# Performance work log

Hardware: AMD Instinct MI355X
Metric: run time of the kernel (lower is better)

## Reference

```python
import jax, jax.numpy as jnp
import numpy as np

B, T, D, H, C = 32, 2048, 64, 512, 10


def setup_inputs() -> dict:
    key = jax.random.key(0)
    ks = jax.random.split(key, 7)
    s_ih = 1.0 / np.sqrt(H)
    return {
        "x": jax.random.normal(ks[0], (B, T, D), dtype=jnp.float32),
        # PyTorch GRU params: gates ordered (r, z, n)
        "w_ih": jax.random.uniform(ks[1], (3 * H, D), jnp.float32, -s_ih, s_ih),
        "w_hh": jax.random.uniform(ks[2], (3 * H, H), jnp.float32, -s_ih, s_ih),
        "b_ih": jax.random.uniform(ks[3], (3 * H,), jnp.float32, -s_ih, s_ih),
        "b_hh": jax.random.uniform(ks[4], (3 * H,), jnp.float32, -s_ih, s_ih),
        "w_fc": jax.random.uniform(ks[5], (C, H), jnp.float32, -s_ih, s_ih),
        "b_fc": jax.random.uniform(ks[6], (C,), jnp.float32, -s_ih, s_ih),
    }


def _gru_seq(x, w_ih, w_hh, b_ih, b_hh):
    # Precompute input-to-hidden gates for all timesteps: [B,T,3H] -> [T,B,3H]
    gx = jnp.einsum("btd,gd->btg", x, w_ih) + b_ih
    gx = jnp.swapaxes(gx, 0, 1)
    h0 = jnp.zeros((x.shape[0], w_hh.shape[1]), dtype=x.dtype)

    def step(h, gxt):
        gh = h @ w_hh.T + b_hh  # [B,3H]
        gx_r, gx_z, gx_n = jnp.split(gxt, 3, axis=-1)
        gh_r, gh_z, gh_n = jnp.split(gh, 3, axis=-1)
        r = jax.nn.sigmoid(gx_r + gh_r)
        z = jax.nn.sigmoid(gx_z + gh_z)
        n = jnp.tanh(gx_n + r * gh_n)
        h_new = (1.0 - z) * n + z * h
        return h_new, h_new

    _, hs = jax.lax.scan(step, h0, gx)  # hs: [T,B,H]
    return jnp.swapaxes(hs, 0, 1)  # [B,T,H]


def reference(x, w_ih, w_hh, b_ih, b_hh, w_fc, b_fc):
    out = _gru_seq(x, w_ih, w_hh, b_ih, b_hh)
    return jnp.einsum("bth,ch->btc", out, w_fc) + b_fc
```

## Files before the change

### kernel.cpp

```cpp
#include <hip/hip_runtime.h>
#include <cstdint>
#include <cstddef>

#define Bsz 32
#define Tn  2048
#define Dn  64
#define Hn  512
#define Cn  10
#define NDOM 16
#define NGB  16
#define UG   32
#define BPG  2
#define NTH  1024
#define RW   1024
#define PSTR 68

__device__ __forceinline__ float sigmoidf_(float v) { return 1.f / (1.f + __expf(-v)); }
__device__ __forceinline__ float tanhf_(float v) {
  const float c = fminf(fmaxf(v, -15.f), 15.f);
  const float e = __expf(-2.f * c);
  return (1.f - e) / (1.f + e);
}


__global__ __launch_bounds__(NTH) void gru_main(
    const float* __restrict__ x, const float* __restrict__ w_ih,
    const float* __restrict__ w_hh, const float* __restrict__ b_ih,
    const float* __restrict__ b_hh, float* __restrict__ hs,
    unsigned long long* __restrict__ xch)
{
  const int dom  = blockIdx.x & (NDOM - 1);
  const int g    = blockIdx.x >> 4;
  const int tid  = threadIdx.x;
  const int wave = tid >> 6;
  const int lane = tid & 63;
  const int u    = tid & 31;
  const int ksec = tid >> 5;

  __shared__ float hTb[2][1024];
  __shared__ float xT[2][128];
  __shared__ float part[64 * PSTR];

  float wreg[3][16];
  float wxreg[3][2];
  float brz0 = 0.f, brz1 = 0.f, bnx = 0.f, bnh = 0.f;
  #pragma unroll
  for (int i = 0; i < 3; ++i) {
    const int grow = i * Hn + g * UG + u;
    const float4* wp = (const float4*)(w_hh + (size_t)grow * Hn + ksec * 16);
    #pragma unroll
    for (int q = 0; q < 4; ++q) {
      const float4 v = wp[q];
      wreg[i][q * 4 + 0] = v.x; wreg[i][q * 4 + 1] = v.y;
      wreg[i][q * 4 + 2] = v.z; wreg[i][q * 4 + 3] = v.w;
    }
    wxreg[i][0] = w_ih[(size_t)grow * Dn + ksec * 2 + 0];
    wxreg[i][1] = w_ih[(size_t)grow * Dn + ksec * 2 + 1];
    if (i == 0) brz0 = b_ih[grow] + b_hh[grow];
    else if (i == 1) brz1 = b_ih[grow] + b_hh[grow];
    else { bnx = b_ih[grow]; bnh = b_hh[grow]; }
  }

  unsigned long long* const sl0 = xch + (size_t)dom * RW;
  unsigned long long* const sl1 = xch + (size_t)(NDOM + dom) * RW;

  const bool dopoll = (wave < 15);
  int wword = 0;
  if (dopoll) {
    const int idx = wave * 64 + lane;
    wword = (idx < g * 64) ? idx : idx + 64;
  }
  const int ownw = g * 64 + (lane & 31) * 2 + (lane >> 5);

  hTb[0][tid & 1023] = 0.f;
  if (tid < 128) {
    const int bp = tid >> 6, d = tid & 63;
    xT[0][d * 2 + bp] = x[((size_t)(dom * BPG + bp) * Tn + 0) * Dn + d];
  }
  float hold = 0.f;
  __syncthreads();

  for (int t = 0; t < Tn; ++t) {
    const int tp = t & 1;
    float* const hT = hTb[tp];
    unsigned long long* const slot = tp ? sl0 : sl1;

    const unsigned long long want = (unsigned long long)t;
    unsigned long long v = 0;
    if (t > 0 && dopoll)
      v = __hip_atomic_load(slot + wword, __ATOMIC_RELAXED, __HIP_MEMORY_SCOPE_AGENT);

    float xpre = 0.f;
    if (tid < 128) {
      const int bp = tid >> 6, d = tid & 63;
      const int tn = (t + 1 < Tn) ? (t + 1) : t;
      xpre = x[((size_t)(dom * BPG + bp) * Tn + tn) * Dn + d];
    }

    float acc[4][2];
    #pragma unroll
    for (int i = 0; i < 4; ++i) { acc[i][0] = 0.f; acc[i][1] = 0.f; }
    #pragma unroll
    for (int dd = 0; dd < 2; ++dd) {
      const float2 xb = *(const float2*)&xT[tp][(ksec * 2 + dd) * 2];
      #pragma unroll
      for (int i = 0; i < 3; ++i) {
        const float w = wxreg[i][dd];
        const int gi = (i == 2) ? 2 : i;
        acc[gi][0] += w * xb.x; acc[gi][1] += w * xb.y;
      }
    }

    if (dopoll) {
      if (t > 0) {
        int gd = 0;
        while ((v >> 32) != want) {
          v = __hip_atomic_load(slot + wword, __ATOMIC_RELAXED, __HIP_MEMORY_SCOPE_AGENT);
          if (++gd > (1 << 17)) break;
        }
        union { unsigned u32; float f; } c;
        c.u32 = (unsigned)v;
        hT[wword] = c.f;
      }
    } else if (t > 0) {
      const float4* pp = (const float4*)&part[lane * PSTR];
      float4 s = pp[0];
      #pragma unroll
      for (int w = 1; w < 16; ++w) {
        const float4 pv = pp[w];
        s.x += pv.x; s.y += pv.y; s.z += pv.z; s.w += pv.w;
      }
      const float r = sigmoidf_(s.x + brz0);
      const float z = sigmoidf_(s.y + brz1);
      const float n = tanhf_(s.z + bnx + r * (s.w + bnh));
      const float h = (1.f - z) * n + z * hold;
      hold = h;
      hT[ownw] = h;
      union { float f; unsigned u32; } cu; cu.f = h;
      asm volatile("s_waitcnt vmcnt(0)" ::: "memory");
      const unsigned long long w64 = (want << 32) | cu.u32;
      __hip_atomic_store(slot + ownw, w64, __ATOMIC_RELAXED, __HIP_MEMORY_SCOPE_AGENT);
      hs[((size_t)(t - 1) * NDOM + dom) * RW + ownw] = h;
    }

    if (tid < 128) { const int bp = tid >> 6, d = tid & 63; xT[tp ^ 1][d * 2 + bp] = xpre; }

    asm volatile("s_waitcnt lgkmcnt(0)" ::: "memory");
    __builtin_amdgcn_s_barrier();
    asm volatile("" ::: "memory");

    {
      const float* hp = hT + ksec * 32;
      #pragma unroll
      for (int k2 = 0; k2 < 8; ++k2) {
        const float4 hv = *(const float4*)(hp + k2 * 4);
        const float a0 = wreg[0][k2 * 2], a1 = wreg[0][k2 * 2 + 1];
        const float b0 = wreg[1][k2 * 2], b1 = wreg[1][k2 * 2 + 1];
        const float c0 = wreg[2][k2 * 2], c1 = wreg[2][k2 * 2 + 1];
        acc[0][0] += a0 * hv.x; acc[0][1] += a0 * hv.y;
        acc[0][0] += a1 * hv.z; acc[0][1] += a1 * hv.w;
        acc[1][0] += b0 * hv.x; acc[1][1] += b0 * hv.y;
        acc[1][0] += b1 * hv.z; acc[1][1] += b1 * hv.w;
        acc[3][0] += c0 * hv.x; acc[3][1] += c0 * hv.y;
        acc[3][0] += c1 * hv.z; acc[3][1] += c1 * hv.w;
      }
    }

    #pragma unroll
    for (int i = 0; i < 4; ++i) {
      acc[i][0] += __shfl_xor(acc[i][0], 32);
      acc[i][1] += __shfl_xor(acc[i][1], 32);
    }

    if (lane < 32) {
      float4 p0, p1;
      p0.x = acc[0][0]; p0.y = acc[1][0]; p0.z = acc[2][0]; p0.w = acc[3][0];
      p1.x = acc[0][1]; p1.y = acc[1][1]; p1.z = acc[2][1]; p1.w = acc[3][1];
      *(float4*)&part[u * PSTR + wave * 4]        = p0;
      *(float4*)&part[(32 + u) * PSTR + wave * 4] = p1;
    }

    asm volatile("s_waitcnt lgkmcnt(0)" ::: "memory");
    __builtin_amdgcn_s_barrier();
    asm volatile("" ::: "memory");
  }

  if (wave == 15) {
    const float4* pp = (const float4*)&part[lane * PSTR];
    float4 s = pp[0];
    #pragma unroll
    for (int w = 1; w < 16; ++w) {
      const float4 pv = pp[w];
      s.x += pv.x; s.y += pv.y; s.z += pv.z; s.w += pv.w;
    }
    const float r = sigmoidf_(s.x + brz0);
    const float z = sigmoidf_(s.y + brz1);
    const float n = tanhf_(s.z + bnx + r * (s.w + bnh));
    const float h = (1.f - z) * n + z * hold;
    hs[((size_t)(Tn - 1) * NDOM + dom) * RW + ownw] = h;
  }
}

__global__ __launch_bounds__(256) void gru_fc(const float* __restrict__ hs,
    const float* __restrict__ w_fc, const float* __restrict__ b_fc,
    float* __restrict__ out)
{
  __shared__ float wfc[Cn * Hn];
  const int tid = threadIdx.x;
  for (int i = tid; i < Cn * Hn; i += 256) wfc[i] = w_fc[i];
  __syncthreads();
  const int wave = tid >> 6, lane = tid & 63;
  const int bt = blockIdx.x * 4 + wave;
  const int b = bt >> 11, t = bt & (Tn - 1);
  const int dom = b >> 1, bp = b & 1;
  const float* src = hs + ((size_t)t * NDOM + dom) * RW;
  float acc[Cn];
  #pragma unroll
  for (int c = 0; c < Cn; ++c) acc[c] = 0.f;
  #pragma unroll
  for (int it = 0; it < 8; ++it) {
    const int unit = it * 64 + lane;
    const float h = src[unit * 2 + bp];
    #pragma unroll
    for (int c = 0; c < Cn; ++c) acc[c] += h * wfc[c * Hn + unit];
  }
  #pragma unroll
  for (int c = 0; c < Cn; ++c) {
    #pragma unroll
    for (int m = 1; m < 64; m <<= 1) acc[c] += __shfl_xor(acc[c], m);
  }
  if (lane == 0) {
    #pragma unroll
    for (int c = 0; c < Cn; ++c) out[(size_t)bt * Cn + c] = acc[c] + b_fc[c];
  }
}

__global__ __launch_bounds__(512) void gru_fallback(
    const float* __restrict__ x, const float* __restrict__ w_ih,
    const float* __restrict__ w_hh, const float* __restrict__ b_ih,
    const float* __restrict__ b_hh, const float* __restrict__ w_fc,
    const float* __restrict__ b_fc, float* __restrict__ out)
{
  const int b = blockIdx.x;
  const int tid = threadIdx.x;
  __shared__ float hsh[Hn];
  __shared__ float xsh[Dn];
  hsh[tid] = 0.f;
  __syncthreads();
  for (int t = 0; t < Tn; ++t) {
    if (tid < Dn) xsh[tid] = x[((size_t)b * Tn + t) * Dn + tid];
    __syncthreads();
    const int u = tid;
    float gxr = 0.f, gxz = 0.f, gxn = 0.f;
    for (int d = 0; d < Dn; ++d) {
      const float xv = xsh[d];
      gxr += w_ih[(size_t)u * Dn + d] * xv;
      gxz += w_ih[(size_t)(Hn + u) * Dn + d] * xv;
      gxn += w_ih[(size_t)(2 * Hn + u) * Dn + d] * xv;
    }
    float ghr = 0.f, ghz = 0.f, ghn = 0.f;
    for (int k = 0; k < Hn; ++k) {
      const float hv = hsh[k];
      ghr += w_hh[(size_t)u * Hn + k] * hv;
      ghz += w_hh[(size_t)(Hn + u) * Hn + k] * hv;
      ghn += w_hh[(size_t)(2 * Hn + u) * Hn + k] * hv;
    }
    const float r = sigmoidf_(gxr + b_ih[u] + ghr + b_hh[u]);
    const float z = sigmoidf_(gxz + b_ih[Hn + u] + ghz + b_hh[Hn + u]);
    const float n = tanhf(gxn + b_ih[2 * Hn + u] + r * (ghn + b_hh[2 * Hn + u]));
    const float hold = hsh[u];
    __syncthreads();
    hsh[u] = (1.f - z) * n + z * hold;
    __syncthreads();
    if (tid < 320) {
      const int c = tid >> 5, l = tid & 31;
      float a = 0.f;
      for (int kk = 0; kk < 16; ++kk) {
        const int j = l * 16 + kk;
        a += hsh[j] * w_fc[c * Hn + j];
      }
      a += __shfl_xor(a, 1); a += __shfl_xor(a, 2); a += __shfl_xor(a, 4);
      a += __shfl_xor(a, 8); a += __shfl_xor(a, 16);
      if (l == 0) out[((size_t)b * Tn + t) * Cn + c] = a + b_fc[c];
    }
    __syncthreads();
  }
}

extern "C" void kernel_launch(void* const* d_in, const int* in_sizes, int n_in,
                              void* d_out, int out_size, void* d_ws, size_t ws_size,
                              hipStream_t stream) {
  const float* x    = (const float*)d_in[0];
  const float* w_ih = (const float*)d_in[1];
  const float* w_hh = (const float*)d_in[2];
  const float* b_ih = (const float*)d_in[3];
  const float* b_hh = (const float*)d_in[4];
  const float* w_fc = (const float*)d_in[5];
  const float* b_fc = (const float*)d_in[6];
  float* out = (float*)d_out;

  const size_t hs_bytes  = (size_t)Tn * NDOM * RW * sizeof(float);
  const size_t xch_bytes = (size_t)2 * NDOM * RW * sizeof(unsigned long long);

  if (ws_size >= hs_bytes) {
    float* hs = (float*)d_ws;
    unsigned long long* xchg = (unsigned long long*)d_out;
    hipMemsetAsync(xchg, 0, xch_bytes, stream);
    hipLaunchKernelGGL(gru_main, dim3(NDOM * NGB), dim3(NTH), 0, stream,
                       x, w_ih, w_hh, b_ih, b_hh, hs, xchg);
    hipLaunchKernelGGL(gru_fc, dim3((Bsz * Tn) / 4), dim3(256), 0, stream,
                       hs, w_fc, b_fc, out);
  } else {
    hipLaunchKernelGGL(gru_fallback, dim3(Bsz), dim3(512), 0, stream,
                       x, w_ih, w_hh, b_ih, b_hh, w_fc, b_fc, out);
  }
}
```

Before: 5.479 ms.

## Merge two per-step barriers into one by double-buffering partials

The GRU recurrence loop now uses a single block barrier per timestep instead of two. Partial gate sums are double-buffered in shared memory, and the hidden vector goes to one shared buffer. Wave 15 reduces the previous step's partials and publishes its own h slice first, then every wave, including wave 15, polls global memory for the full h vector. This shortens the serial critical path per step but depends on subtle ordering: hT is rewritten without a barrier separating it from the previous step's reads, so there is a risk of races.

```diff
diff --git a/kernel.cpp b/kernel.cpp
--- a/kernel.cpp
+++ b/kernel.cpp
@@ -13,7 +13,6 @@
 #define BPG  2
 #define NTH  1024
 #define RW   1024
-#define PSTR 68
 
 __device__ __forceinline__ float sigmoidf_(float v) { return 1.f / (1.f + __expf(-v)); }
 __device__ __forceinline__ float tanhf_(float v) {
@@ -37,9 +36,9 @@
   const int u    = tid & 31;
   const int ksec = tid >> 5;
 
-  __shared__ float hTb[2][1024];
+  __shared__ float hT[1024];
   __shared__ float xT[2][128];
-  __shared__ float part[64 * PSTR];
+  __shared__ float part[2][4096];
 
   float wreg[3][16];
   float wxreg[3][2];
@@ -64,31 +63,46 @@
   unsigned long long* const sl0 = xch + (size_t)dom * RW;
   unsigned long long* const sl1 = xch + (size_t)(NDOM + dom) * RW;
 
-  const bool dopoll = (wave < 15);
-  int wword = 0;
-  if (dopoll) {
-    const int idx = wave * 64 + lane;
-    wword = (idx < g * 64) ? idx : idx + 64;
-  }
-  const int ownw = g * 64 + (lane & 31) * 2 + (lane >> 5);
-
-  hTb[0][tid & 1023] = 0.f;
+  const int wword = wave * 64 + lane;
+  const int ownw  = g * 64 + (lane & 31) * 2 + (lane >> 5);
+
+  hT[tid] = 0.f;
   if (tid < 128) {
     const int bp = tid >> 6, d = tid & 63;
     xT[0][d * 2 + bp] = x[((size_t)(dom * BPG + bp) * Tn + 0) * Dn + d];
   }
-  float hold = 0.f;
+  float hold = 0.f, hsave = 0.f;
   __syncthreads();
 
   for (int t = 0; t < Tn; ++t) {
     const int tp = t & 1;
-    float* const hT = hTb[tp];
     unsigned long long* const slot = tp ? sl0 : sl1;
-
     const unsigned long long want = (unsigned long long)t;
+
     unsigned long long v = 0;
-    if (t > 0 && dopoll)
+    if (t > 0) {
+      if (wave == 15) {
+        const float* pb = part[tp ^ 1];
+        float s0 = 0.f, s1 = 0.f, s2 = 0.f, s3 = 0.f;
+        #pragma unroll
+        for (int w = 0; w < 16; ++w) {
+          s0 += pb[       w * 64 + lane];
+          s1 += pb[1024 + w * 64 + lane];
+          s2 += pb[2048 + w * 64 + lane];
+          s3 += pb[3072 + w * 64 + lane];
+        }
+        const float r = sigmoidf_(s0 + brz0);
+        const float z = sigmoidf_(s1 + brz1);
+        const float n = tanhf_(s2 + bnx + r * (s3 + bnh));
+        const float h = (1.f - z) * n + z * hold;
+        hold = h; hsave = h;
+        union { float f; unsigned u32; } cu; cu.f = h;
+        asm volatile("s_waitcnt vmcnt(0)" ::: "memory");
+        __hip_atomic_store(slot + ownw, (want << 32) | cu.u32,
+                           __ATOMIC_RELAXED, __HIP_MEMORY_SCOPE_AGENT);
+      }
       v = __hip_atomic_load(slot + wword, __ATOMIC_RELAXED, __HIP_MEMORY_SCOPE_AGENT);
+    }
 
     float xpre = 0.f;
     if (tid < 128) {
@@ -111,43 +125,19 @@
       }
     }
 
-    if (dopoll) {
-      if (t > 0) {
-        int gd = 0;
-        while ((v >> 32) != want) {
-          v = __hip_atomic_load(slot + wword, __ATOMIC_RELAXED, __HIP_MEMORY_SCOPE_AGENT);
-          if (++gd > (1 << 17)) break;
-        }
-        union { unsigned u32; float f; } c;
-        c.u32 = (unsigned)v;
-        hT[wword] = c.f;
-      }
-    } else if (t > 0) {
-      const float4* pp = (const float4*)&part[lane * PSTR];
-      float4 s = pp[0];
-      #pragma unroll
-      for (int w = 1; w < 16; ++w) {
-        const float4 pv = pp[w];
-        s.x += pv.x; s.y += pv.y; s.z += pv.z; s.w += pv.w;
-      }
-      const float r = sigmoidf_(s.x + brz0);
-      const float z = sigmoidf_(s.y + brz1);
-      const float n = tanhf_(s.z + bnx + r * (s.w + bnh));
-      const float h = (1.f - z) * n + z * hold;
-      hold = h;
-      hT[ownw] = h;
-      union { float f; unsigned u32; } cu; cu.f = h;
-      asm volatile("s_waitcnt vmcnt(0)" ::: "memory");
-      const unsigned long long w64 = (want << 32) | cu.u32;
-      __hip_atomic_store(slot + ownw, w64, __ATOMIC_RELAXED, __HIP_MEMORY_SCOPE_AGENT);
-      hs[((size_t)(t - 1) * NDOM + dom) * RW + ownw] = h;
+    if (t > 0) {
+      int gd = 0;
+      while ((v >> 32) != want) {
+        v = __hip_atomic_load(slot + wword, __ATOMIC_RELAXED, __HIP_MEMORY_SCOPE_AGENT);
+        if (++gd > (1 << 17)) break;
+      }
+      union { unsigned u32; float f; } c; c.u32 = (unsigned)v;
+      hT[wword] = c.f;
     }
 
     if (tid < 128) { const int bp = tid >> 6, d = tid & 63; xT[tp ^ 1][d * 2 + bp] = xpre; }
 
     asm volatile("s_waitcnt lgkmcnt(0)" ::: "memory");
-    __builtin_amdgcn_s_barrier();
-    asm volatile("" ::: "memory");
 
     {
       const float* hp = hT + ksec * 32;
@@ -172,13 +162,17 @@
       acc[i][1] += __shfl_xor(acc[i][1], 32);
     }
 
-    if (lane < 32) {
-      float4 p0, p1;
-      p0.x = acc[0][0]; p0.y = acc[1][0]; p0.z = acc[2][0]; p0.w = acc[3][0];
-      p1.x = acc[0][1]; p1.y = acc[1][1]; p1.z = acc[2][1]; p1.w = acc[3][1];
-      *(float4*)&part[u * PSTR + wave * 4]        = p0;
-      *(float4*)&part[(32 + u) * PSTR + wave * 4] = p1;
-    }
+    {
+      float* pb = part[tp];
+      const int b = lane >> 5;
+      pb[       wave * 64 + lane] = acc[0][b];
+      pb[1024 + wave * 64 + lane] = acc[1][b];
+      pb[2048 + wave * 64 + lane] = acc[2][b];
+      pb[3072 + wave * 64 + lane] = acc[3][b];
+    }
+
+    if (wave == 15 && t > 0)
+      hs[((size_t)(t - 1) * NDOM + dom) * RW + ownw] = hsave;
 
     asm volatile("s_waitcnt lgkmcnt(0)" ::: "memory");
     __builtin_amdgcn_s_barrier();
@@ -186,16 +180,18 @@
   }
 
   if (wave == 15) {
-    const float4* pp = (const float4*)&part[lane * PSTR];
-    float4 s = pp[0];
-    #pragma unroll
-    for (int w = 1; w < 16; ++w) {
-      const float4 pv = pp[w];
-      s.x += pv.x; s.y += pv.y; s.z += pv.z; s.w += pv.w;
-    }
-    const float r = sigmoidf_(s.x + brz0);
-    const float z = sigmoidf_(s.y + brz1);
-    const float n = tanhf_(s.z + bnx + r * (s.w + bnh));
+    const float* pb = part[(Tn - 1) & 1];
+    float s0 = 0.f, s1 = 0.f, s2 = 0.f, s3 = 0.f;
+    #pragma unroll
+    for (int w = 0; w < 16; ++w) {
+      s0 += pb[       w * 64 + lane];
+      s1 += pb[1024 + w * 64 + lane];
+      s2 += pb[2048 + w * 64 + lane];
+      s3 += pb[3072 + w * 64 + lane];
+    }
+    const float r = sigmoidf_(s0 + brz0);
+    const float z = sigmoidf_(s1 + brz1);
+    const float n = tanhf_(s2 + bnx + r * (s3 + bnh));
     const float h = (1.f - z) * n + z * hold;
     hs[((size_t)(Tn - 1) * NDOM + dom) * RW + ownw] = h;
   }
```

New measurement: 9.654 ms. +76.2%, slower.
